# Kernel optimization log

Hardware: AMD Instinct MI355X
Metric: run time of the kernel (lower is better)

## Reference

```python
import jax, jax.numpy as jnp
import numpy as np

B, T, D = 1024, 12, 512


def setup_inputs() -> dict:
    key = jax.random.key(0)
    k1, k2 = jax.random.split(key)
    predictions = jax.random.normal(k1, (B, T, D), dtype=jnp.float32)
    x_future_encoded = jax.random.normal(k2, (B, T, D), dtype=jnp.float32)
    return {"predictions": predictions, "x_future_encoded": x_future_encoded}


def reference(predictions, x_future_encoded):
    # predictions, x_future_encoded: [B, T, D]
    b, t, _ = predictions.shape
    # dot[t, i, j] = <x_future_encoded[i, t], predictions[j, t]>  (matmul with transpose_b)
    dots = jnp.einsum('itd,jtd->tij', x_future_encoded, predictions)  # [T, B, B]
    # log_softmax over axis=0 of each [B, B] slice -> axis=1 of [T, B, B]
    log_sm = jax.nn.log_softmax(dots, axis=1)
    diag = jnp.diagonal(log_sm, axis1=1, axis2=2)          # [T, B]
    losses = jnp.sum(diag, axis=0) / t                      # [B]
    loss = jnp.mean(losses)
    # argmax of softmax(axis=0) == argmax of logits over axis=0
    pred_idx = jnp.argmax(dots, axis=1)                     # [T, B]
    correct = (pred_idx == jnp.arange(b)[None, :]).astype(jnp.float32)
    accuracy = jnp.mean(correct)  # == mean over t of count_nonzero/B
    return (-1.0 * loss, accuracy)
```

## Files before the change

### kernel.cpp

```cpp
#include <hip/hip_runtime.h>
#include <cstdint>
#include <cstddef>

#define Bsz 1024
#define Tsz 12
#define Dsz 512

#define NIB 16
#define NKS 16

typedef _Float16 f16x8 __attribute__((ext_vector_type(8)));
typedef float    f32x4 __attribute__((ext_vector_type(4)));

__device__ __forceinline__ f16x8 cvt8(const f32x4 v0, const f32x4 v1) {
    f16x8 h;
#pragma unroll
    for (int e = 0; e < 4; ++e) {
        h[e]     = (_Float16)v0[e];
        h[e + 4] = (_Float16)v1[e];
    }
    return h;
}

__global__ __launch_bounds__(256) void convert_kernel(
    const float* __restrict__ P, const float* __restrict__ X,
    _Float16* __restrict__ Af, _Float16* __restrict__ Bf,
    float* __restrict__ out)
{
    if (blockIdx.x == 0 && blockIdx.y == 0 && blockIdx.z == 0 && threadIdx.x < 2)
        out[threadIdx.x] = 0.0f;

    const int tid  = threadIdx.x;
    const int w    = tid >> 6;
    const int lane = tid & 63;
    const int rb   = blockIdx.x >> 2;
    const int ks   = ((blockIdx.x & 3) << 2) + w;
    const int t    = blockIdx.y;
    const int arr  = blockIdx.z;

    const float* src = arr ? X : P;
    _Float16*    dst = arr ? Bf : Af;

    const int bl   = lane >> 2;
    const int doct = lane & 3;
    const float* s = src + ((size_t)(rb * 16 + bl) * Tsz + t) * Dsz
                   + (size_t)ks * 32 + doct * 8;
    const f32x4 v0 = *(const f32x4*)s;
    const f32x4 v1 = *(const f32x4*)(s + 4);

    const int lo = bl + (doct << 4);
    _Float16* dp = dst + ((((size_t)t * 64 + rb) * 16 + ks) * 64 + lo) * 8;
    *(f16x8*)dp = cvt8(v0, v1);
}

__global__ __launch_bounds__(256, 3) void gemm_fused_kernel(
    const _Float16* __restrict__ Af,
    const _Float16* __restrict__ Bf,
    float* __restrict__ pm,
    float* __restrict__ ps,
    int*   __restrict__ pa,
    float* __restrict__ diag)
{
    const int orig = blockIdx.x + (blockIdx.y << 2) + (blockIdx.z << 6);
    const int wgid = (orig & 7) * 96 + (orig >> 3);
    const int t      = wgid >> 6;
    const int rem    = wgid & 63;
    const int jstrip = rem >> 2;
    const int ic     = rem & 3;
    const int jb  = jstrip * 64;

    const int tid  = threadIdx.x;
    const int lane = tid & 63;
    const int w    = tid >> 6;
    const int ibw  = ic * 256 + w * 64;
    const int ml   = lane & 15;
    const int quad = lane >> 4;

    f32x4 acc[4][4];
#pragma unroll
    for (int r = 0; r < 4; ++r)
#pragma unroll
        for (int c = 0; c < 4; ++c) acc[r][c] = (f32x4){0.f, 0.f, 0.f, 0.f};

    const _Float16* Ap = Af + ((size_t)(t * 64 + (jb  >> 4)) * 16 * 64 + lane) * 8;
    const _Float16* Bp = Bf + ((size_t)(t * 64 + (ibw >> 4)) * 16 * 64 + lane) * 8;

#pragma unroll 4
    for (int ks = 0; ks < NKS; ++ks) {
        f16x8 ah[4], bh[4];
#pragma unroll
        for (int r = 0; r < 4; ++r)
            ah[r] = *(const f16x8*)(Ap + (size_t)(r * 16 + ks) * 512);
#pragma unroll
        for (int c = 0; c < 4; ++c)
            bh[c] = *(const f16x8*)(Bp + (size_t)(c * 16 + ks) * 512);

#pragma unroll
        for (int r = 0; r < 4; ++r)
#pragma unroll
            for (int c = 0; c < 4; ++c)
                acc[r][c] = __builtin_amdgcn_mfma_f32_16x16x32_f16(ah[r], bh[c], acc[r][c], 0, 0, 0);
    }

#pragma unroll
    for (int r = 0; r < 4; ++r)
#pragma unroll
        for (int v = 0; v < 4; ++v) {
            const int jg = jb + r * 16 + quad * 4 + v;
#pragma unroll
            for (int c = 0; c < 4; ++c) {
                const int ig = ibw + c * 16 + ml;
                if (ig == jg) diag[(size_t)t * Bsz + jg] = acc[r][c][v];
            }
        }

#pragma unroll
    for (int r = 0; r < 4; ++r)
#pragma unroll
        for (int v = 0; v < 4; ++v) {
            float m = acc[r][0][v];
            int   ai = ml;
#pragma unroll
            for (int c = 1; c < 4; ++c) {
                const float val = acc[r][c][v];
                if (val > m) { m = val; ai = c * 16 + ml; }
            }
#pragma unroll
            for (int off = 1; off < 16; off <<= 1) {
                const float om = __shfl_xor(m, off);
                const int   oi = __shfl_xor(ai, off);
                if (om > m || (om == m && oi < ai)) { m = om; ai = oi; }
            }
            float s = 0.0f;
#pragma unroll
            for (int c = 0; c < 4; ++c) s += __expf(acc[r][c][v] - m);
#pragma unroll
            for (int off = 1; off < 16; off <<= 1) s += __shfl_xor(s, off);

            if (ml == 0) {
                const int row = jb + r * 16 + quad * 4 + v;
                const size_t slot = ((size_t)t * Bsz + row) * NIB + (ibw >> 6);
                pm[slot] = m;
                ps[slot] = s;
                pa[slot] = ibw + ai;
            }
        }
}

__global__ __launch_bounds__(256) void combine_kernel(
    const float* __restrict__ pm,
    const float* __restrict__ ps,
    const int*   __restrict__ pa,
    const float* __restrict__ diag,
    float* __restrict__ out)
{
    const int col = blockIdx.x * 256 + threadIdx.x;
    const int j = col & (Bsz - 1);

    const size_t base = (size_t)col * NIB;
    float M = pm[base]; int A = pa[base];
#pragma unroll
    for (int b = 1; b < NIB; ++b) {
        const float mb = pm[base + b];
        if (mb > M) { M = mb; A = pa[base + b]; }
    }
    float S = 0.0f;
#pragma unroll
    for (int b = 0; b < NIB; ++b) S += ps[base + b] * __expf(pm[base + b] - M);

    const float lse = M + logf(S);
    float sl = lse - diag[col];
    float sc = (A == j) ? 1.0f : 0.0f;

#pragma unroll
    for (int off = 1; off < 64; off <<= 1) {
        sl += __shfl_xor(sl, off);
        sc += __shfl_xor(sc, off);
    }

    __shared__ float wl[4], wc[4];
    const int w = threadIdx.x >> 6;
    if ((threadIdx.x & 63) == 0) { wl[w] = sl; wc[w] = sc; }
    __syncthreads();
    if (threadIdx.x == 0) {
        const float inv = 1.0f / (float)(Bsz * Tsz);
        atomicAdd(&out[0], (wl[0] + wl[1] + wl[2] + wl[3]) * inv);
        atomicAdd(&out[1], (wc[0] + wc[1] + wc[2] + wc[3]) * inv);
    }
}

extern "C" void kernel_launch(void* const* d_in, const int* in_sizes, int n_in,
                              void* d_out, int out_size, void* d_ws, size_t ws_size,
                              hipStream_t stream) {
    const float* P = (const float*)d_in[0];
    const float* X = (const float*)d_in[1];
    float* out = (float*)d_out;

    const size_t ncol  = (size_t)Bsz * Tsz;
    const size_t nslot = ncol * NIB;
    const size_t nel   = (size_t)Bsz * Tsz * Dsz;

    float* pm   = (float*)d_ws;
    float* ps   = pm + nslot;
    int*   pa   = (int*)(ps + nslot);
    float* diag = (float*)(pa + nslot);
    _Float16* Af = (_Float16*)(diag + ncol);
    _Float16* Bf = Af + nel;

    convert_kernel<<<dim3(256, Tsz, 2), dim3(256), 0, stream>>>(P, X, Af, Bf, out);

    gemm_fused_kernel<<<dim3(4, 16, Tsz), dim3(256), 0, stream>>>(
        Af, Bf, pm, ps, pa, diag);

    combine_kernel<<<dim3((int)(ncol / 256)), dim3(256), 0, stream>>>(
        pm, ps, pa, diag, out);
}
```

Baseline: 115.1 us.

## Fuse fp32-to-fp16 conversion into GEMM kernel, dropping separate convert pass

Removes the standalone convert kernel that repacked P and X into an MFMA-friendly fp16 layout. The GEMM now loads fp32 rows directly from the original [B,T,D] layout and converts to fp16 in registers before each MFMA. This saves one kernel launch and the write and re-read of the fp16 copies. In exchange each GEMM workgroup reads twice as many bytes per operand, with less coalesced strided row accesses. Inputs are also re-read across the four column blocks that share them, and the unroll factor drops to 2.

```diff
diff --git a/kernel.cpp b/kernel.cpp
--- a/kernel.cpp
+++ b/kernel.cpp
@@ -22,44 +22,14 @@
     return h;
 }
 
-__global__ __launch_bounds__(256) void convert_kernel(
-    const float* __restrict__ P, const float* __restrict__ X,
-    _Float16* __restrict__ Af, _Float16* __restrict__ Bf,
-    float* __restrict__ out)
-{
-    if (blockIdx.x == 0 && blockIdx.y == 0 && blockIdx.z == 0 && threadIdx.x < 2)
-        out[threadIdx.x] = 0.0f;
-
-    const int tid  = threadIdx.x;
-    const int w    = tid >> 6;
-    const int lane = tid & 63;
-    const int rb   = blockIdx.x >> 2;
-    const int ks   = ((blockIdx.x & 3) << 2) + w;
-    const int t    = blockIdx.y;
-    const int arr  = blockIdx.z;
-
-    const float* src = arr ? X : P;
-    _Float16*    dst = arr ? Bf : Af;
-
-    const int bl   = lane >> 2;
-    const int doct = lane & 3;
-    const float* s = src + ((size_t)(rb * 16 + bl) * Tsz + t) * Dsz
-                   + (size_t)ks * 32 + doct * 8;
-    const f32x4 v0 = *(const f32x4*)s;
-    const f32x4 v1 = *(const f32x4*)(s + 4);
-
-    const int lo = bl + (doct << 4);
-    _Float16* dp = dst + ((((size_t)t * 64 + rb) * 16 + ks) * 64 + lo) * 8;
-    *(f16x8*)dp = cvt8(v0, v1);
-}
-
 __global__ __launch_bounds__(256, 3) void gemm_fused_kernel(
-    const _Float16* __restrict__ Af,
-    const _Float16* __restrict__ Bf,
+    const float* __restrict__ P,
+    const float* __restrict__ X,
     float* __restrict__ pm,
     float* __restrict__ ps,
     int*   __restrict__ pa,
-    float* __restrict__ diag)
+    float* __restrict__ diag,
+    float* __restrict__ out)
 {
     const int orig = blockIdx.x + (blockIdx.y << 2) + (blockIdx.z << 6);
     const int wgid = (orig & 7) * 96 + (orig >> 3);
@@ -76,24 +46,31 @@
     const int ml   = lane & 15;
     const int quad = lane >> 4;
 
+    if (orig == 0 && tid < 2) out[tid] = 0.0f;
+
     f32x4 acc[4][4];
 #pragma unroll
     for (int r = 0; r < 4; ++r)
 #pragma unroll
         for (int c = 0; c < 4; ++c) acc[r][c] = (f32x4){0.f, 0.f, 0.f, 0.f};
 
-    const _Float16* Ap = Af + ((size_t)(t * 64 + (jb  >> 4)) * 16 * 64 + lane) * 8;
-    const _Float16* Bp = Bf + ((size_t)(t * 64 + (ibw >> 4)) * 16 * 64 + lane) * 8;
+    const size_t strideRow = (size_t)Tsz * Dsz;
+    const float* Pb = P + ((size_t)(jb  + ml) * Tsz + t) * Dsz + quad * 8;
+    const float* Xb = X + ((size_t)(ibw + ml) * Tsz + t) * Dsz + quad * 8;
 
-#pragma unroll 4
+#pragma unroll 2
     for (int ks = 0; ks < NKS; ++ks) {
         f16x8 ah[4], bh[4];
 #pragma unroll
-        for (int r = 0; r < 4; ++r)
-            ah[r] = *(const f16x8*)(Ap + (size_t)(r * 16 + ks) * 512);
+        for (int r = 0; r < 4; ++r) {
+            const float* s = Pb + (size_t)r * 16 * strideRow + ks * 32;
+            ah[r] = cvt8(*(const f32x4*)s, *(const f32x4*)(s + 4));
+        }
 #pragma unroll
-        for (int c = 0; c < 4; ++c)
-            bh[c] = *(const f16x8*)(Bp + (size_t)(c * 16 + ks) * 512);
+        for (int c = 0; c < 4; ++c) {
+            const float* s = Xb + (size_t)c * 16 * strideRow + ks * 32;
+            bh[c] = cvt8(*(const f32x4*)s, *(const f32x4*)(s + 4));
+        }
 
 #pragma unroll
         for (int r = 0; r < 4; ++r)
@@ -198,19 +175,14 @@
 
     const size_t ncol  = (size_t)Bsz * Tsz;
     const size_t nslot = ncol * NIB;
-    const size_t nel   = (size_t)Bsz * Tsz * Dsz;
 
     float* pm   = (float*)d_ws;
     float* ps   = pm + nslot;
     int*   pa   = (int*)(ps + nslot);
     float* diag = (float*)(pa + nslot);
-    _Float16* Af = (_Float16*)(diag + ncol);
-    _Float16* Bf = Af + nel;
-
-    convert_kernel<<<dim3(256, Tsz, 2), dim3(256), 0, stream>>>(P, X, Af, Bf, out);
 
     gemm_fused_kernel<<<dim3(4, 16, Tsz), dim3(256), 0, stream>>>(
-        Af, Bf, pm, ps, pa, diag);
+        P, X, pm, ps, pa, diag, out);
 
     combine_kernel<<<dim3((int)(ncol / 256)), dim3(256), 0, stream>>>(
         pm, ps, pa, diag, out);
```

New measurement: 174.5 us. 1.52x slower.
